# Kernel optimization log

Measured on AMD Instinct MI355X. Metric: run time of the kernel, lower is better.

The kernel has to match this reference:

```python
import jax, jax.numpy as jnp
import numpy as np

# ---- dims (from init_kwargs) ----
B_SZ = 16; K = 1; NC = 64; NR = 4; RF = 4; L_UL = 8
M_ANT = 256; N_ANT = 1024; BS_TDD = 16; RIS_TDD = 16
FC = 100e9; BW = 1e9; UPSNR = 10.0; MAX_DELAY = 5e-9; BIT = 1
C = NC  # PSA channel = Nc


def setup_inputs():
    key = jax.random.key(0)
    ks = jax.random.split(key, 20)
    f = jnp.float32
    d = {}
    d['H_BR_re'] = jax.random.normal(ks[0], (NC, N_ANT, M_ANT), f)
    d['H_BR_im'] = jax.random.normal(ks[1], (NC, N_ANT, M_ANT), f)
    d['H_RU_re'] = jax.random.normal(ks[2], (B_SZ, K, NC, NR, N_ANT), f)
    d['H_RU_im'] = jax.random.normal(ks[3], (B_SZ, K, NC, NR, N_ANT), f)
    d['H_BU_re'] = jax.random.normal(ks[4], (B_SZ, K, NC, NR, M_ANT), f)
    d['H_BU_im'] = jax.random.normal(ks[5], (B_SZ, K, NC, NR, M_ANT), f)
    # unit complex Gaussian noise, scaled by sqrt(Power*SNR/2) inside reference
    d['noise_re'] = jax.random.normal(ks[6], (B_SZ, L_UL, NC, NR, RF), f)
    d['noise_im'] = jax.random.normal(ks[7], (B_SZ, L_UL, NC, NR, RF), f)
    # learned parameters (torch: Parameter tensors in __init__)
    d['Phase1'] = jax.random.uniform(ks[8], (L_UL, N_ANT), f)
    d['Phase2'] = jax.random.uniform(ks[9], (L_UL, N_ANT), f)
    d['Phase_TDD'] = jax.random.normal(ks[10], (L_UL, RIS_TDD), f)
    d['S_analog'] = jax.random.normal(ks[11], (L_UL, NC, M_ANT, RF), f)
    d['S_analog_TDD'] = jax.random.normal(ks[12], (L_UL, NC, BS_TDD, RF), f)
    # ParallelPolarizedSelfAttention(channel=Nc) weights (1x1 convs -> [out,in])
    s = 0.05
    d['ch_wv_w'] = jax.random.normal(ks[13], (C // 2, C), f) * s
    d['ch_wv_b'] = jnp.zeros((C // 2,), f)
    d['ch_wq_w'] = jax.random.normal(ks[14], (1, C), f) * s
    d['ch_wq_b'] = jnp.zeros((1,), f)
    d['ch_wz_w'] = jax.random.normal(ks[15], (C, C // 2), f) * s
    d['ch_wz_b'] = jnp.zeros((C,), f)
    d['ln_w'] = jnp.ones((C,), f)
    d['ln_b'] = jnp.zeros((C,), f)
    d['sp_wv_w'] = jax.random.normal(ks[16], (C // 2, C), f) * s
    d['sp_wv_b'] = jnp.zeros((C // 2,), f)
    d['sp_wq_w'] = jax.random.normal(ks[17], (C // 2, C), f) * s
    d['sp_wq_b'] = jnp.zeros((C // 2,), f)
    return d


def _conv1x1(x, w, b):
    # 1x1 conv == channel mixing
    return jnp.einsum('bchw,oc->bohw', x, w) + b[None, :, None, None]


def _psa(x, ch_wv_w, ch_wv_b, ch_wq_w, ch_wq_b, ch_wz_w, ch_wz_b, ln_w, ln_b,
         sp_wv_w, sp_wv_b, sp_wq_w, sp_wq_b):
    # Parallel Polarized Self-Attention (channel branch + spatial branch)
    b, c, h, w = x.shape
    # channel-only self-attention
    cwv = _conv1x1(x, ch_wv_w, ch_wv_b).reshape(b, c // 2, h * w)
    cwq = jax.nn.softmax(_conv1x1(x, ch_wq_w, ch_wq_b).reshape(b, h * w), axis=1)
    cwz = jnp.einsum('bkn,bn->bk', cwv, cwq)          # [b, c//2]
    z = cwz @ ch_wz_w.T + ch_wz_b                      # [b, c]
    mu = jnp.mean(z, axis=-1, keepdims=True)
    var = jnp.var(z, axis=-1, keepdims=True)
    zn = (z - mu) / jnp.sqrt(var + 1e-5) * ln_w + ln_b  # LayerNorm over channel
    ch_weight = jax.nn.sigmoid(zn)[:, :, None, None]
    # spatial-only self-attention
    swv = _conv1x1(x, sp_wv_w, sp_wv_b).reshape(b, c // 2, h * w)
    swq = jax.nn.softmax(jnp.mean(_conv1x1(x, sp_wq_w, sp_wq_b), axis=(2, 3)), axis=-1)
    swz = jnp.einsum('bk,bkn->bn', swq, swv)
    sp_weight = jax.nn.sigmoid(swz.reshape(b, 1, h, w))
    return sp_weight * x + ch_weight * x


def reference(H_BR_re, H_BR_im, H_RU_re, H_RU_im, H_BU_re, H_BU_im,
              noise_re, noise_im, Phase1, Phase2, Phase_TDD, S_analog, S_analog_TDD,
              ch_wv_w, ch_wv_b, ch_wq_w, ch_wq_b, ch_wz_w, ch_wz_b, ln_w, ln_b,
              sp_wv_w, sp_wv_b, sp_wq_w, sp_wq_b):
    H_BR = H_BR_re + 1j * H_BR_im                       # [Nc, N_ant, M_ant]
    H_RU = H_RU_re[:, K - 1] + 1j * H_RU_im[:, K - 1]   # [B, Nc, Nr, N_ant]
    H_BU = H_BU_re[:, K - 1] + 1j * H_BU_im[:, K - 1]   # [B, Nc, Nr, M_ant]
    two_pi = 2.0 * jnp.pi
    # subcarrier frequencies fm = (n - (Nc+1)/2) * B/Nc + fc
    fm = ((jnp.arange(NC, dtype=jnp.float32) + 1.0) - (NC + 1) / 2.0) * (BW / NC) + FC
    # phase quantization (bit = 1 -> seg = pi)
    seg = two_pi / (2 ** BIT)
    th1 = jnp.exp(1j * (jnp.floor(two_pi * Phase1 / seg) * seg))  # [L, N_ant]
    th2 = jnp.exp(1j * (jnp.floor(two_pi * Phase2 / seg) * seg))  # [L, N_ant]
    # RIS true-time-delay phase, kron(Phi_T, ones(1, N_ant//RIS_TDD)) == repeat
    a1 = MAX_DELAY * jax.nn.sigmoid(Phase_TDD)                    # [L, RIS_TDD]
    phi_t = jnp.exp(1j * two_pi * fm[None, :, None] * a1[:, None, :])
    phi_tdd = jnp.repeat(phi_t, N_ANT // RIS_TDD, axis=-1)        # [L, Nc, N_ant]
    theta = th1[:, None, :] * phi_tdd * th2[:, None, :]           # diag(Theta) entries
    # BS analog precoder with TTDs; kron(S_T, ones(M//BS_TDD,1)) == row repeat
    S = jnp.exp(1j * S_analog) / float(np.sqrt(M_ANT))            # [L, Nc, M, RF]
    bdel = MAX_DELAY * jax.nn.sigmoid(S_analog_TDD)               # [L, Nc, BS_TDD, RF]
    s_t = jnp.exp(1j * two_pi * fm[None, :, None, None] * bdel)
    F = S * jnp.repeat(s_t, M_ANT // BS_TDD, axis=2)              # [L, Nc, M, RF]
    # H_RU @ diag(theta) == column-wise scaling (fused, no NxN diag matmul)
    scaled = H_RU[:, None] * theta[None, :, :, None, :]           # [B, L, Nc, Nr, N_ant]
    a = jnp.einsum('blcrn,cnm->blcrm', scaled, H_BR) + H_BU[:, None]
    y0 = jnp.einsum('blcrm,lcmf->blcrf', a, F)                    # [B, L, Nc, Nr, RF]
    power = jnp.sum(jnp.abs(y0) ** 2, axis=(3, 4))[..., None, None]
    snr_lin = 10.0 ** (-UPSNR / 10.0)
    noise = (noise_re + 1j * noise_im) * jnp.sqrt(power * snr_lin / 2.0)
    y = y0 + noise
    Y = jnp.transpose(y, (0, 2, 3, 4, 1)).reshape(B_SZ, NC, K * NR * RF, L_UL)
    x = jnp.concatenate([jnp.real(Y), jnp.imag(Y)], axis=3)       # [B, Nc, K*Nr*RF, 2L]
    return _psa(x, ch_wv_w, ch_wv_b, ch_wq_w, ch_wq_b, ch_wz_w, ch_wz_b,
                ln_w, ln_b, sp_wv_w, sp_wv_b, sp_wq_w, sp_wq_b)
```

## Files before the change

### kernel.cpp

```cpp
#include <hip/hip_runtime.h>
#include <math.h>

static constexpr double TWO_PI_D = 6.283185307179586476925287;

static constexpr size_t OFF_THRE = 0;
static constexpr size_t OFF_THIM = 524288;
static constexpr size_t OFF_FBF  = 1048576;
static constexpr size_t OFF_WTBF = 1572864;
static constexpr size_t OFF_Y0P  = 3670016;
static constexpr size_t OFF_X    = 4980736;
static constexpr size_t WS_FLOATS = 5242880;

typedef __attribute__((ext_vector_type(8))) short short8;
typedef __attribute__((ext_vector_type(4))) float f32x4;

__device__ __forceinline__ double fm_of(int c){
  return ((double)(c + 1) - 32.5) * (1.0e9 / 64.0) + 1.0e11;
}
__device__ __forceinline__ unsigned short f2bf(float x){
  unsigned int u = __float_as_uint(x);
  return (unsigned short)((u + 0x7FFFu + ((u >> 16) & 1u)) >> 16);
}

__global__ __launch_bounds__(256) void k_prep(
    const float* __restrict__ P1, const float* __restrict__ P2,
    const float* __restrict__ PT, const float* __restrict__ SA,
    const float* __restrict__ ST,
    float* __restrict__ tre, float* __restrict__ tim, unsigned short* __restrict__ Fbf)
{
  __shared__ double tcs[16], tsn[16];
  int bid = blockIdx.x, tid = threadIdx.x;
  const float TWO_PI_F = 6.2831855f, SEG_F = 3.1415927f;
  if (bid < 2048){
    int l = bid >> 8, c = (bid >> 2) & 63, n0 = (bid & 3) * 256;
    if (tid < 4){
      int ris = (n0 >> 6) + tid;
      double a1 = 5.0e-9 / (1.0 + exp((double)(-PT[l * 16 + ris])));
      sincos(TWO_PI_D * fm_of(c) * a1, &tsn[tid], &tcs[tid]);
    }
    __syncthreads();
    int n = n0 + tid;
    float p1 = P1[l * 1024 + n], p2 = P2[l * 1024 + n];
    int k1 = (int)floorf((TWO_PI_F * p1) / SEG_F);
    int k2 = (int)floorf((TWO_PI_F * p2) / SEG_F);
    float s = ((k1 + k2) & 1) ? -1.f : 1.f;
    int t = (l * 64 + c) * 1024 + n;
    int ti = tid >> 6;
    tre[t] = s * (float)tcs[ti];
    tim[t] = s * (float)tsn[ti];
  } else {
    int bid2 = bid - 2048;
    int l = bid2 >> 8, c = (bid2 >> 2) & 63, f = bid2 & 3;
    int m = tid;
    if (tid < 16){
      double bdel = 5.0e-9 / (1.0 + exp((double)(-ST[((l * 64 + c) * 16 + tid) * 4 + f])));
      sincos(TWO_PI_D * fm_of(c) * bdel, &tsn[tid], &tcs[tid]);
    }
    __syncthreads();
    float sa_ = SA[(size_t)((l * 64 + c) * 256 + m) * 4 + f];
    float ssa, csa;
    sincosf(sa_, &ssa, &csa);
    float cb = (float)tcs[m >> 4], sb = (float)tsn[m >> 4];
    size_t base = ((size_t)(c * 2) * 32 + (l * 4 + f)) * 256 + m;
    Fbf[base]        = f2bf((csa * cb - ssa * sb) * 0.0625f);
    Fbf[base + 8192] = f2bf((csa * sb + ssa * cb) * 0.0625f);
  }
}

__global__ __launch_bounds__(256) void k_W(
    const float* __restrict__ Hre, const float* __restrict__ Him,
    const unsigned short* __restrict__ Fbf,
    const float* __restrict__ tre, const float* __restrict__ tim,
    unsigned short* __restrict__ WTbf)
{
  const int bid = blockIdx.x;
  const int c = bid >> 4;
  const int n0 = (bid & 15) * 64;
  const int lane = threadIdx.x & 63, w = threadIdx.x >> 6;
  const int nt = n0 + w * 16;
  const int kq = lane >> 4, rm = lane & 15;

  const size_t arow = ((size_t)c * 1024 + nt + rm) * 256 + kq * 8;
  const float* hr = Hre + arow;
  const float* hi = Him + arow;
  const unsigned short* f0 = Fbf + (size_t)(c * 2) * 8192 + kq * 8;
  const unsigned short* fr0 = f0 + rm * 256;
  const unsigned short* fi0 = fr0 + 8192;
  const unsigned short* fr1 = f0 + (16 + rm) * 256;
  const unsigned short* fi1 = fr1 + 8192;

  f32x4 accRe0 = {0.f,0.f,0.f,0.f}, accIm0 = {0.f,0.f,0.f,0.f};
  f32x4 accRe1 = {0.f,0.f,0.f,0.f}, accIm1 = {0.f,0.f,0.f,0.f};

  #pragma unroll
  for (int ck = 0; ck < 8; ck++){
    const int mo = ck * 32;
    float4 r0 = *(const float4*)(hr + mo);
    float4 r1 = *(const float4*)(hr + mo + 4);
    float4 i0 = *(const float4*)(hi + mo);
    float4 i1 = *(const float4*)(hi + mo + 4);
    short8 bRe0 = *(const short8*)(fr0 + mo);
    short8 bIm0 = *(const short8*)(fi0 + mo);
    short8 bRe1 = *(const short8*)(fr1 + mo);
    short8 bIm1 = *(const short8*)(fi1 + mo);
    short8 are, aim;
    are[0]=(short)f2bf(r0.x); are[1]=(short)f2bf(r0.y); are[2]=(short)f2bf(r0.z); are[3]=(short)f2bf(r0.w);
    are[4]=(short)f2bf(r1.x); are[5]=(short)f2bf(r1.y); are[6]=(short)f2bf(r1.z); are[7]=(short)f2bf(r1.w);
    aim[0]=(short)f2bf(i0.x); aim[1]=(short)f2bf(i0.y); aim[2]=(short)f2bf(i0.z); aim[3]=(short)f2bf(i0.w);
    aim[4]=(short)f2bf(i1.x); aim[5]=(short)f2bf(i1.y); aim[6]=(short)f2bf(i1.z); aim[7]=(short)f2bf(i1.w);
    short8 bImN0, bImN1;
    #pragma unroll
    for (int j = 0; j < 8; j++){
      bImN0[j] = bIm0[j] ^ (short)0x8000;
      bImN1[j] = bIm1[j] ^ (short)0x8000;
    }
    accRe0 = __builtin_amdgcn_mfma_f32_16x16x32_bf16(are, bRe0,  accRe0, 0, 0, 0);
    accRe0 = __builtin_amdgcn_mfma_f32_16x16x32_bf16(aim, bImN0, accRe0, 0, 0, 0);
    accIm0 = __builtin_amdgcn_mfma_f32_16x16x32_bf16(are, bIm0,  accIm0, 0, 0, 0);
    accIm0 = __builtin_amdgcn_mfma_f32_16x16x32_bf16(aim, bRe0,  accIm0, 0, 0, 0);
    accRe1 = __builtin_amdgcn_mfma_f32_16x16x32_bf16(are, bRe1,  accRe1, 0, 0, 0);
    accRe1 = __builtin_amdgcn_mfma_f32_16x16x32_bf16(aim, bImN1, accRe1, 0, 0, 0);
    accIm1 = __builtin_amdgcn_mfma_f32_16x16x32_bf16(are, bIm1,  accIm1, 0, 0, 0);
    accIm1 = __builtin_amdgcn_mfma_f32_16x16x32_bf16(aim, bRe1,  accIm1, 0, 0, 0);
  }

  #pragma unroll
  for (int t = 0; t < 2; t++){
    const f32x4 aR = t ? accRe1 : accRe0;
    const f32x4 aI = t ? accIm1 : accIm0;
    int lf = t * 16 + rm;
    int l = lf >> 2;
    unsigned short pr[4], pi_[4];
    #pragma unroll
    for (int r = 0; r < 4; r++){
      size_t ti = (size_t)(l * 64 + c) * 1024 + nt + kq * 4 + r;
      float wr = tre[ti], wi = tim[ti];
      float xr = aR[r], xi = aI[r];
      pr[r]  = f2bf(wr * xr - wi * xi);
      pi_[r] = f2bf(wr * xi + wi * xr);
    }
    size_t rb = ((size_t)(c * 2) * 32 + lf) * 1024 + nt + kq * 4;
    *(uint2*)(WTbf + rb) =
        make_uint2((unsigned)pr[0] | ((unsigned)pr[1] << 16),
                   (unsigned)pr[2] | ((unsigned)pr[3] << 16));
    *(uint2*)(WTbf + rb + 32768) =
        make_uint2((unsigned)pi_[0] | ((unsigned)pi_[1] << 16),
                   (unsigned)pi_[2] | ((unsigned)pi_[3] << 16));
  }
}

__global__ __launch_bounds__(512) void k_y0(
    const float* __restrict__ Rre, const float* __restrict__ Rim,
    const float* __restrict__ Ure, const float* __restrict__ Uim,
    const unsigned short* __restrict__ WTbf, const unsigned short* __restrict__ Fbf,
    float* __restrict__ Y0p)
{
  __shared__ __align__(16) short lA[2][2][64][32];
  __shared__ __align__(16) short lB[2][2][32][32];
  const int bid = blockIdx.x;
  const int chunk = bid >> 6, c = bid & 63;
  const int tid = threadIdx.x;
  const int lane = tid & 63, w = tid >> 6;
  const int lftile = w & 1, mt = w >> 1;
  const int kq = lane >> 4, rm = lane & 15;
  const int s_mq = tid & 7, s_nr = tid >> 3;
  const int b_comp = tid >> 7, b_lf = (tid >> 2) & 31, b_q = tid & 3;

  const float* Are; const float* Aim; int ars, ac0;
  const unsigned short* Bb; int brs;
  if (chunk < 4){ Are = Rre; Aim = Rim; ars = 1024; ac0 = chunk * 256; Bb = WTbf; brs = 1024; }
  else          { Are = Ure; Aim = Uim; ars = 256;  ac0 = 0;           Bb = Fbf;  brs = 256;  }
  const size_t arow = ((size_t)((s_nr >> 2) * 64 + c) * 4 + (s_nr & 3)) * ars + ac0;

  f32x4 accRe = {0.f,0.f,0.f,0.f}, accIm = {0.f,0.f,0.f,0.f};
  float4 sRe, sIm; short8 sB;

  auto LOADC = [&](int ck){
    size_t g = arow + ck * 32 + s_mq * 4;
    sRe = *(const float4*)(Are + g);
    sIm = *(const float4*)(Aim + g);
    if (tid < 256){
      size_t gb = ((size_t)(c * 2 + b_comp) * 32 + b_lf) * brs + ac0 + ck * 32 + b_q * 8;
      sB = *(const short8*)(Bb + gb);
    }
  };
  auto WRITEC = [&](int buf){
    int eo = (((s_mq >> 1) ^ (s_nr & 3)) << 3) + (s_mq & 1) * 4;
    unsigned int r0 = (unsigned)f2bf(sRe.x) | ((unsigned)f2bf(sRe.y) << 16);
    unsigned int r1 = (unsigned)f2bf(sRe.z) | ((unsigned)f2bf(sRe.w) << 16);
    *(uint2*)&lA[buf][0][s_nr][eo] = make_uint2(r0, r1);
    unsigned int i0 = (unsigned)f2bf(sIm.x) | ((unsigned)f2bf(sIm.y) << 16);
    unsigned int i1 = (unsigned)f2bf(sIm.z) | ((unsigned)f2bf(sIm.w) << 16);
    *(uint2*)&lA[buf][1][s_nr][eo] = make_uint2(i0, i1);
    if (tid < 256){
      *(short8*)&lB[buf][b_comp][b_lf][(b_q ^ (b_lf & 3)) << 3] = sB;
    }
  };
  auto COMPUTE = [&](int buf){
    int col = lftile * 16 + rm;
    int be = (kq ^ (col & 3)) << 3;
    short8 bRe = *(const short8*)&lB[buf][0][col][be];
    short8 bIm = *(const short8*)&lB[buf][1][col][be];
    short8 bImN;
    #pragma unroll
    for (int i = 0; i < 8; i++) bImN[i] = bIm[i] ^ (short)0x8000;
    int row = mt * 16 + rm;
    int eo = (kq ^ (row & 3)) << 3;
    short8 are = *(const short8*)&lA[buf][0][row][eo];
    short8 aim = *(const short8*)&lA[buf][1][row][eo];
    accRe = __builtin_amdgcn_mfma_f32_16x16x32_bf16(are, bRe,  accRe, 0, 0, 0);
    accRe = __builtin_amdgcn_mfma_f32_16x16x32_bf16(aim, bImN, accRe, 0, 0, 0);
    accIm = __builtin_amdgcn_mfma_f32_16x16x32_bf16(are, bIm,  accIm, 0, 0, 0);
    accIm = __builtin_amdgcn_mfma_f32_16x16x32_bf16(aim, bRe,  accIm, 0, 0, 0);
  };

  LOADC(0); WRITEC(0); __syncthreads();
  for (int ck = 0; ck < 8; ck++){
    int buf = ck & 1;
    if (ck < 7) LOADC(ck + 1);
    COMPUTE(buf);
    if (ck < 7) WRITEC(buf ^ 1);
    __syncthreads();
  }

  #pragma unroll
  for (int r = 0; r < 4; r++){
    int row = mt * 16 + kq * 4 + r;
    int lf = lftile * 16 + rm;
    size_t idx = ((size_t)(chunk * 64 + c) * 64 + row) * 32 + lf;
    float2 o; o.x = accRe[r]; o.y = accIm[r];
    *(float2*)(Y0p + idx * 2) = o;
  }
}

__global__ __launch_bounds__(256) void k_fin(
    const float* __restrict__ Y0p,
    const float* __restrict__ nre, const float* __restrict__ nim,
    float* __restrict__ X)
{
  int wid = blockIdx.x * 4 + (threadIdx.x >> 6);
  int lane = threadIdx.x & 63;
  int c = wid & 63, l = (wid >> 6) & 7, b = wid >> 9;
  int pair = lane >> 2;
  int r = pair >> 2, f = pair & 3;
  float yR = 0.f, yI = 0.f;
  #pragma unroll
  for (int ch = 0; ch < 5; ch++){
    size_t idx = ((size_t)(ch * 64 + c) * 64 + b * 4 + r) * 32 + l * 4 + f;
    float2 v = *(const float2*)(Y0p + idx * 2);
    yR += v.x; yI += v.y;
  }
  float p = yR * yR + yI * yI;
  p += __shfl_xor(p, 4); p += __shfl_xor(p, 8);
  p += __shfl_xor(p, 16); p += __shfl_xor(p, 32);
  float sc = sqrtf(p * 0.05f);
  if ((lane & 3) == 0){
    size_t ni = ((size_t)((b * 8 + l) * 64 + c) * 4 + r) * 4 + f;
    float oR = yR + nre[ni] * sc;
    float oI = yI + nim[ni] * sc;
    size_t xb = ((size_t)(b * 64 + c) * 16 + pair) * 16;
    X[xb + l]     = oR;
    X[xb + 8 + l] = oI;
  }
}

__global__ __launch_bounds__(256) void k_psa(
    const float* __restrict__ Xin,
    const float* __restrict__ wv_w, const float* __restrict__ wv_b,
    const float* __restrict__ wq_w, const float* __restrict__ wq_b,
    const float* __restrict__ wz_w, const float* __restrict__ wz_b,
    const float* __restrict__ lnw, const float* __restrict__ lnb,
    const float* __restrict__ sv_w, const float* __restrict__ sv_b,
    const float* __restrict__ sq_w, const float* __restrict__ sq_b,
    float* __restrict__ out)
{
  __shared__ float x[64 * 257];
  __shared__ float buf[256];
  __shared__ float xms[64], xqs[64], chw[64], wcomb[64];
  __shared__ float cwzs[32], swqs[32];
  __shared__ float red4[8];
  int b = blockIdx.x, tid = threadIdx.x;
  const float* xin = Xin + (size_t)b * 16384;
  for (int kk = 0; kk < 64; kk++){
    int i = tid + 256 * kk;
    x[(i >> 8) * 257 + (i & 255)] = xin[i];
  }
  __syncthreads();
  if (tid < 64){
    float s = 0.f;
    for (int n = 0; n < 256; n++) s += x[tid * 257 + n];
    xms[tid] = s * (1.f / 256.f);
  }
  float lq = wq_b[0];
  for (int cc = 0; cc < 64; cc++) lq += wq_w[cc] * x[cc * 257 + tid];
  float mx = lq;
  for (int s = 1; s < 64; s <<= 1) mx = fmaxf(mx, __shfl_xor(mx, s));
  if ((tid & 63) == 0) red4[tid >> 6] = mx;
  __syncthreads();
  mx = fmaxf(fmaxf(red4[0], red4[1]), fmaxf(red4[2], red4[3]));
  float e = expf(lq - mx);
  float se = e;
  for (int s = 1; s < 64; s <<= 1) se += __shfl_xor(se, s);
  if ((tid & 63) == 0) red4[4 + (tid >> 6)] = se;
  __syncthreads();
  se = red4[4] + red4[5] + red4[6] + red4[7];
  buf[tid] = e / se;
  __syncthreads();
  if (tid < 64){
    float s = 0.f;
    for (int n = 0; n < 256; n++) s += x[tid * 257 + n] * buf[n];
    xqs[tid] = s;
  }
  __syncthreads();
  if (tid < 32){
    float s = wv_b[tid];
    for (int cc = 0; cc < 64; cc++) s += wv_w[tid * 64 + cc] * xqs[cc];
    cwzs[tid] = s;
  }
  __syncthreads();
  if (tid < 64){
    float z = wz_b[tid];
    for (int k = 0; k < 32; k++) z += cwzs[k] * wz_w[tid * 32 + k];
    float s1 = z, s2 = z * z;
    for (int s = 1; s < 64; s <<= 1){ s1 += __shfl_xor(s1, s); s2 += __shfl_xor(s2, s); }
    float mu = s1 * (1.f / 64.f);
    float var = s2 * (1.f / 64.f) - mu * mu;
    float zn = (z - mu) * rsqrtf(var + 1e-5f) * lnw[tid] + lnb[tid];
    chw[tid] = 1.f / (1.f + expf(-zn));
  }
  if (tid < 32){
    float s = sq_b[tid];
    for (int cc = 0; cc < 64; cc++) s += sq_w[tid * 64 + cc] * xms[cc];
    float m2 = s;
    for (int st = 1; st < 32; st <<= 1) m2 = fmaxf(m2, __shfl_xor(m2, st));
    float ee = expf(s - m2), ss = ee;
    for (int st = 1; st < 32; st <<= 1) ss += __shfl_xor(ss, st);
    swqs[tid] = ee / ss;
  }
  __syncthreads();
  if (tid < 64){
    float s = 0.f;
    for (int k = 0; k < 32; k++) s += swqs[k] * sv_w[k * 64 + tid];
    wcomb[tid] = s;
  }
  __syncthreads();
  float bcomb = 0.f;
  for (int k = 0; k < 32; k++) bcomb += swqs[k] * sv_b[k];
  float sz = bcomb;
  for (int cc = 0; cc < 64; cc++) sz += wcomb[cc] * x[cc * 257 + tid];
  float spw = 1.f / (1.f + expf(-sz));
  buf[tid] = spw;
  __syncthreads();
  for (int kk = 0; kk < 64; kk++){
    int i = tid + 256 * kk;
    int cc = i >> 8, n = i & 255;
    out[(size_t)b * 16384 + i] = (buf[n] + chw[cc]) * x[cc * 257 + n];
  }
}

extern "C" void kernel_launch(void* const* d_in, const int* in_sizes, int n_in,
                              void* d_out, int out_size, void* d_ws, size_t ws_size,
                              hipStream_t stream)
{
  if (ws_size < WS_FLOATS * sizeof(float)) return;
  const float* HBRre = (const float*)d_in[0];
  const float* HBRim = (const float*)d_in[1];
  const float* HRUre = (const float*)d_in[2];
  const float* HRUim = (const float*)d_in[3];
  const float* HBUre = (const float*)d_in[4];
  const float* HBUim = (const float*)d_in[5];
  const float* nre   = (const float*)d_in[6];
  const float* nim   = (const float*)d_in[7];
  const float* P1    = (const float*)d_in[8];
  const float* P2    = (const float*)d_in[9];
  const float* PT    = (const float*)d_in[10];
  const float* SA    = (const float*)d_in[11];
  const float* ST    = (const float*)d_in[12];
  const float* wv_w  = (const float*)d_in[13];
  const float* wv_b  = (const float*)d_in[14];
  const float* wq_w  = (const float*)d_in[15];
  const float* wq_b  = (const float*)d_in[16];
  const float* wz_w  = (const float*)d_in[17];
  const float* wz_b  = (const float*)d_in[18];
  const float* lnw   = (const float*)d_in[19];
  const float* lnb   = (const float*)d_in[20];
  const float* sv_w  = (const float*)d_in[21];
  const float* sv_b  = (const float*)d_in[22];
  const float* sq_w  = (const float*)d_in[23];
  const float* sq_b  = (const float*)d_in[24];

  float* ws  = (float*)d_ws;
  float* tre = ws + OFF_THRE;
  float* tim = ws + OFF_THIM;
  unsigned short* fbf  = (unsigned short*)(ws + OFF_FBF);
  unsigned short* wtbf = (unsigned short*)(ws + OFF_WTBF);
  float* y0p = ws + OFF_Y0P;
  float* xb  = ws + OFF_X;

  k_prep<<<4096, 256, 0, stream>>>(P1, P2, PT, SA, ST, tre, tim, fbf);
  k_W<<<1024, 256, 0, stream>>>(HBRre, HBRim, fbf, tre, tim, wtbf);
  k_y0<<<320, 512, 0, stream>>>(HRUre, HRUim, HBUre, HBUim, wtbf, fbf, y0p);
  k_fin<<<2048, 256, 0, stream>>>(y0p, nre, nim, xb);
  k_psa<<<16, 256, 0, stream>>>(xb, wv_w, wv_b, wq_w, wq_b, wz_w, wz_b,
                                lnw, lnb, sv_w, sv_b, sq_w, sq_b, (float*)d_out);
}
```

Baseline: 69.98 us.

## Split k_W work per wave across lf tiles and double-buffer K loads

Each wave in k_W now computes a single 16-wide lf tile instead of two, so H rows are shared by two waves and the grid doubles to 2048 blocks over 32-row n chunks. The K loop is hand-pipelined with two register buffer sets, issuing the next chunk's loads before the current chunk's MFMAs. The goal is more parallelism and latency hiding on the memory-bound H_BR read. The cost is that each H_BR element is loaded twice, once per lf tile, which relies on cache to avoid doubling global traffic.

Result: slower. 83.17 us (+18.8%).

```diff
diff --git a/kernel.cpp b/kernel.cpp
--- a/kernel.cpp
+++ b/kernel.cpp
@@ -74,68 +74,81 @@
     unsigned short* __restrict__ WTbf)
 {
   const int bid = blockIdx.x;
-  const int c = bid >> 4;
-  const int n0 = (bid & 15) * 64;
+  const int c = bid >> 5;
+  const int n0 = (bid & 31) * 32;
   const int lane = threadIdx.x & 63, w = threadIdx.x >> 6;
-  const int nt = n0 + w * 16;
+  const int lftile = w & 1, rh = w >> 1;
+  const int nt = n0 + rh * 16;
   const int kq = lane >> 4, rm = lane & 15;
+  const int lf = lftile * 16 + rm;
 
   const size_t arow = ((size_t)c * 1024 + nt + rm) * 256 + kq * 8;
   const float* hr = Hre + arow;
   const float* hi = Him + arow;
-  const unsigned short* f0 = Fbf + (size_t)(c * 2) * 8192 + kq * 8;
-  const unsigned short* fr0 = f0 + rm * 256;
-  const unsigned short* fi0 = fr0 + 8192;
-  const unsigned short* fr1 = f0 + (16 + rm) * 256;
-  const unsigned short* fi1 = fr1 + 8192;
-
-  f32x4 accRe0 = {0.f,0.f,0.f,0.f}, accIm0 = {0.f,0.f,0.f,0.f};
-  f32x4 accRe1 = {0.f,0.f,0.f,0.f}, accIm1 = {0.f,0.f,0.f,0.f};
-
-  #pragma unroll
-  for (int ck = 0; ck < 8; ck++){
-    const int mo = ck * 32;
-    float4 r0 = *(const float4*)(hr + mo);
-    float4 r1 = *(const float4*)(hr + mo + 4);
-    float4 i0 = *(const float4*)(hi + mo);
-    float4 i1 = *(const float4*)(hi + mo + 4);
-    short8 bRe0 = *(const short8*)(fr0 + mo);
-    short8 bIm0 = *(const short8*)(fi0 + mo);
-    short8 bRe1 = *(const short8*)(fr1 + mo);
-    short8 bIm1 = *(const short8*)(fi1 + mo);
-    short8 are, aim;
-    are[0]=(short)f2bf(r0.x); are[1]=(short)f2bf(r0.y); are[2]=(short)f2bf(r0.z); are[3]=(short)f2bf(r0.w);
-    are[4]=(short)f2bf(r1.x); are[5]=(short)f2bf(r1.y); are[6]=(short)f2bf(r1.z); are[7]=(short)f2bf(r1.w);
-    aim[0]=(short)f2bf(i0.x); aim[1]=(short)f2bf(i0.y); aim[2]=(short)f2bf(i0.z); aim[3]=(short)f2bf(i0.w);
-    aim[4]=(short)f2bf(i1.x); aim[5]=(short)f2bf(i1.y); aim[6]=(short)f2bf(i1.z); aim[7]=(short)f2bf(i1.w);
-    short8 bImN0, bImN1;
-    #pragma unroll
-    for (int j = 0; j < 8; j++){
-      bImN0[j] = bIm0[j] ^ (short)0x8000;
-      bImN1[j] = bIm1[j] ^ (short)0x8000;
-    }
-    accRe0 = __builtin_amdgcn_mfma_f32_16x16x32_bf16(are, bRe0,  accRe0, 0, 0, 0);
-    accRe0 = __builtin_amdgcn_mfma_f32_16x16x32_bf16(aim, bImN0, accRe0, 0, 0, 0);
-    accIm0 = __builtin_amdgcn_mfma_f32_16x16x32_bf16(are, bIm0,  accIm0, 0, 0, 0);
-    accIm0 = __builtin_amdgcn_mfma_f32_16x16x32_bf16(aim, bRe0,  accIm0, 0, 0, 0);
-    accRe1 = __builtin_amdgcn_mfma_f32_16x16x32_bf16(are, bRe1,  accRe1, 0, 0, 0);
-    accRe1 = __builtin_amdgcn_mfma_f32_16x16x32_bf16(aim, bImN1, accRe1, 0, 0, 0);
-    accIm1 = __builtin_amdgcn_mfma_f32_16x16x32_bf16(are, bIm1,  accIm1, 0, 0, 0);
-    accIm1 = __builtin_amdgcn_mfma_f32_16x16x32_bf16(aim, bRe1,  accIm1, 0, 0, 0);
-  }
-
-  #pragma unroll
-  for (int t = 0; t < 2; t++){
-    const f32x4 aR = t ? accRe1 : accRe0;
-    const f32x4 aI = t ? accIm1 : accIm0;
-    int lf = t * 16 + rm;
-    int l = lf >> 2;
+  const unsigned short* fr = Fbf + (size_t)c * 16384 + (size_t)lf * 256 + kq * 8;
+  const unsigned short* fi = fr + 8192;
+
+  f32x4 accRe = {0.f,0.f,0.f,0.f}, accIm = {0.f,0.f,0.f,0.f};
+
+  float4 r0A, r1A, i0A, i1A; short8 brA, biA;
+  float4 r0B, r1B, i0B, i1B; short8 brB, biB;
+
+#define LOADK(S, CK) do {                              \
+    const int mo_ = (CK) * 32;                         \
+    r0##S = *(const float4*)(hr + mo_);                \
+    r1##S = *(const float4*)(hr + mo_ + 4);            \
+    i0##S = *(const float4*)(hi + mo_);                \
+    i1##S = *(const float4*)(hi + mo_ + 4);            \
+    br##S = *(const short8*)(fr + mo_);                \
+    bi##S = *(const short8*)(fi + mo_);                \
+  } while (0)
+
+#define COMPK(S) do {                                                                 \
+    short8 are_, aim_, bin_;                                                          \
+    are_[0]=(short)f2bf(r0##S.x); are_[1]=(short)f2bf(r0##S.y);                       \
+    are_[2]=(short)f2bf(r0##S.z); are_[3]=(short)f2bf(r0##S.w);                       \
+    are_[4]=(short)f2bf(r1##S.x); are_[5]=(short)f2bf(r1##S.y);                       \
+    are_[6]=(short)f2bf(r1##S.z); are_[7]=(short)f2bf(r1##S.w);                       \
+    aim_[0]=(short)f2bf(i0##S.x); aim_[1]=(short)f2bf(i0##S.y);                       \
+    aim_[2]=(short)f2bf(i0##S.z); aim_[3]=(short)f2bf(i0##S.w);                       \
+    aim_[4]=(short)f2bf(i1##S.x); aim_[5]=(short)f2bf(i1##S.y);                       \
+    aim_[6]=(short)f2bf(i1##S.z); aim_[7]=(short)f2bf(i1##S.w);                       \
+    _Pragma("unroll")                                                                 \
+    for (int j = 0; j < 8; j++) bin_[j] = bi##S[j] ^ (short)0x8000;                   \
+    accRe = __builtin_amdgcn_mfma_f32_16x16x32_bf16(are_, br##S, accRe, 0, 0, 0);     \
+    accRe = __builtin_amdgcn_mfma_f32_16x16x32_bf16(aim_, bin_,  accRe, 0, 0, 0);     \
+    accIm = __builtin_amdgcn_mfma_f32_16x16x32_bf16(are_, bi##S, accIm, 0, 0, 0);     \
+    accIm = __builtin_amdgcn_mfma_f32_16x16x32_bf16(aim_, br##S, accIm, 0, 0, 0);     \
+  } while (0)
+
+  LOADK(A, 0);
+  LOADK(B, 1);
+  COMPK(A);
+  LOADK(A, 2);
+  COMPK(B);
+  LOADK(B, 3);
+  COMPK(A);
+  LOADK(A, 4);
+  COMPK(B);
+  LOADK(B, 5);
+  COMPK(A);
+  LOADK(A, 6);
+  COMPK(B);
+  LOADK(B, 7);
+  COMPK(A);
+  COMPK(B);
+
+#undef LOADK
+#undef COMPK
+
+  {
+    const int l = lf >> 2;
     unsigned short pr[4], pi_[4];
     #pragma unroll
     for (int r = 0; r < 4; r++){
       size_t ti = (size_t)(l * 64 + c) * 1024 + nt + kq * 4 + r;
       float wr = tre[ti], wi = tim[ti];
-      float xr = aR[r], xi = aI[r];
+      float xr = accRe[r], xi = accIm[r];
       pr[r]  = f2bf(wr * xr - wi * xi);
       pi_[r] = f2bf(wr * xi + wi * xr);
     }
@@ -398,7 +411,7 @@
   float* xb  = ws + OFF_X;
 
   k_prep<<<4096, 256, 0, stream>>>(P1, P2, PT, SA, ST, tre, tim, fbf);
-  k_W<<<1024, 256, 0, stream>>>(HBRre, HBRim, fbf, tre, tim, wtbf);
+  k_W<<<2048, 256, 0, stream>>>(HBRre, HBRim, fbf, tre, tim, wtbf);
   k_y0<<<320, 512, 0, stream>>>(HRUre, HRUim, HBUre, HBUim, wtbf, fbf, y0p);
   k_fin<<<2048, 256, 0, stream>>>(y0p, nre, nim, xb);
   k_psa<<<16, 256, 0, stream>>>(xb, wv_w, wv_b, wq_w, wq_b, wz_w, wz_b,
```

## Stage H_BR tile in LDS via direct global-to-LDS loads and retile k_W

Applied to the files above, without the earlier changes.

k_W now copies each block's 32-row slab of H_BR real/imag (fp32) into padded shared memory with global_load_lds, then has each wave compute one 16x16 output tile from LDS. The block tile shrinks to 32 rows and the grid doubles, with two blocks per CU requested. The aim is coalesced, asynchronous streaming of the large H_BR read, plus more parallelism. In exchange each wave does half the MFMA work per A-load, and LDS use (about 65 KB per block) limits occupancy.

After: 72.09 us. 3.0% more time.

```diff
diff --git a/kernel.cpp b/kernel.cpp
--- a/kernel.cpp
+++ b/kernel.cpp
@@ -13,6 +13,8 @@
 
 typedef __attribute__((ext_vector_type(8))) short short8;
 typedef __attribute__((ext_vector_type(4))) float f32x4;
+typedef __attribute__((address_space(3))) unsigned int lds_u32;
+typedef const __attribute__((address_space(1))) unsigned int glo_u32;
 
 __device__ __forceinline__ double fm_of(int c){
   return ((double)(c + 1) - 32.5) * (1.0e9 / 64.0) + 1.0e11;
@@ -67,75 +69,73 @@
   }
 }
 
-__global__ __launch_bounds__(256) void k_W(
+__global__ __launch_bounds__(256, 2) void k_W(
     const float* __restrict__ Hre, const float* __restrict__ Him,
     const unsigned short* __restrict__ Fbf,
     const float* __restrict__ tre, const float* __restrict__ tim,
     unsigned short* __restrict__ WTbf)
 {
+  __shared__ __align__(16) float lA[16640];
   const int bid = blockIdx.x;
-  const int c = bid >> 4;
-  const int n0 = (bid & 15) * 64;
-  const int lane = threadIdx.x & 63, w = threadIdx.x >> 6;
-  const int nt = n0 + w * 16;
+  const int c = bid >> 5;
+  const int n0 = (bid & 31) * 32;
+  const int tid = threadIdx.x;
+  const int lane = tid & 63, w = tid >> 6;
+
+  const float* hre0 = Hre + ((size_t)c * 1024 + n0) * 256;
+  const float* him0 = Him + ((size_t)c * 1024 + n0) * 256;
+  #pragma unroll
+  for (int i = 0; i < 16; i++){
+    int t = w * 16 + i;
+    int row = t & 31;
+    const float* src = ((t >> 5) ? him0 : hre0) + (size_t)row * 256 + (lane << 2);
+    __builtin_amdgcn_global_load_lds((glo_u32*)src, (lds_u32*)&lA[t * 260], 16, 0, 0);
+  }
+  __syncthreads();
+
+  const int lftile = w & 1, rowhalf = w >> 1;
   const int kq = lane >> 4, rm = lane & 15;
-
-  const size_t arow = ((size_t)c * 1024 + nt + rm) * 256 + kq * 8;
-  const float* hr = Hre + arow;
-  const float* hi = Him + arow;
-  const unsigned short* f0 = Fbf + (size_t)(c * 2) * 8192 + kq * 8;
-  const unsigned short* fr0 = f0 + rm * 256;
-  const unsigned short* fi0 = fr0 + 8192;
-  const unsigned short* fr1 = f0 + (16 + rm) * 256;
-  const unsigned short* fi1 = fr1 + 8192;
-
-  f32x4 accRe0 = {0.f,0.f,0.f,0.f}, accIm0 = {0.f,0.f,0.f,0.f};
-  f32x4 accRe1 = {0.f,0.f,0.f,0.f}, accIm1 = {0.f,0.f,0.f,0.f};
+  const int lf = lftile * 16 + rm;
+  const int rrow = rowhalf * 16 + rm;
+  const int nt = n0 + rowhalf * 16;
+
+  const float* aRe = &lA[rrow * 260 + kq * 8];
+  const float* aIm = aRe + 32 * 260;
+  const unsigned short* fr = Fbf + (size_t)c * 16384 + (size_t)lf * 256 + kq * 8;
+  const unsigned short* fi = fr + 8192;
+
+  f32x4 accRe = {0.f,0.f,0.f,0.f}, accIm = {0.f,0.f,0.f,0.f};
 
   #pragma unroll
   for (int ck = 0; ck < 8; ck++){
     const int mo = ck * 32;
-    float4 r0 = *(const float4*)(hr + mo);
-    float4 r1 = *(const float4*)(hr + mo + 4);
-    float4 i0 = *(const float4*)(hi + mo);
-    float4 i1 = *(const float4*)(hi + mo + 4);
-    short8 bRe0 = *(const short8*)(fr0 + mo);
-    short8 bIm0 = *(const short8*)(fi0 + mo);
-    short8 bRe1 = *(const short8*)(fr1 + mo);
-    short8 bIm1 = *(const short8*)(fi1 + mo);
-    short8 are, aim;
+    float4 r0 = *(const float4*)(aRe + mo);
+    float4 r1 = *(const float4*)(aRe + mo + 4);
+    float4 i0 = *(const float4*)(aIm + mo);
+    float4 i1 = *(const float4*)(aIm + mo + 4);
+    short8 bre = *(const short8*)(fr + mo);
+    short8 bim = *(const short8*)(fi + mo);
+    short8 are, aim, bin;
     are[0]=(short)f2bf(r0.x); are[1]=(short)f2bf(r0.y); are[2]=(short)f2bf(r0.z); are[3]=(short)f2bf(r0.w);
     are[4]=(short)f2bf(r1.x); are[5]=(short)f2bf(r1.y); are[6]=(short)f2bf(r1.z); are[7]=(short)f2bf(r1.w);
     aim[0]=(short)f2bf(i0.x); aim[1]=(short)f2bf(i0.y); aim[2]=(short)f2bf(i0.z); aim[3]=(short)f2bf(i0.w);
     aim[4]=(short)f2bf(i1.x); aim[5]=(short)f2bf(i1.y); aim[6]=(short)f2bf(i1.z); aim[7]=(short)f2bf(i1.w);
-    short8 bImN0, bImN1;
     #pragma unroll
-    for (int j = 0; j < 8; j++){
-      bImN0[j] = bIm0[j] ^ (short)0x8000;
-      bImN1[j] = bIm1[j] ^ (short)0x8000;
-    }
-    accRe0 = __builtin_amdgcn_mfma_f32_16x16x32_bf16(are, bRe0,  accRe0, 0, 0, 0);
-    accRe0 = __builtin_amdgcn_mfma_f32_16x16x32_bf16(aim, bImN0, accRe0, 0, 0, 0);
-    accIm0 = __builtin_amdgcn_mfma_f32_16x16x32_bf16(are, bIm0,  accIm0, 0, 0, 0);
-    accIm0 = __builtin_amdgcn_mfma_f32_16x16x32_bf16(aim, bRe0,  accIm0, 0, 0, 0);
-    accRe1 = __builtin_amdgcn_mfma_f32_16x16x32_bf16(are, bRe1,  accRe1, 0, 0, 0);
-    accRe1 = __builtin_amdgcn_mfma_f32_16x16x32_bf16(aim, bImN1, accRe1, 0, 0, 0);
-    accIm1 = __builtin_amdgcn_mfma_f32_16x16x32_bf16(are, bIm1,  accIm1, 0, 0, 0);
-    accIm1 = __builtin_amdgcn_mfma_f32_16x16x32_bf16(aim, bRe1,  accIm1, 0, 0, 0);
-  }
-
-  #pragma unroll
-  for (int t = 0; t < 2; t++){
-    const f32x4 aR = t ? accRe1 : accRe0;
-    const f32x4 aI = t ? accIm1 : accIm0;
-    int lf = t * 16 + rm;
-    int l = lf >> 2;
+    for (int j = 0; j < 8; j++) bin[j] = bim[j] ^ (short)0x8000;
+    accRe = __builtin_amdgcn_mfma_f32_16x16x32_bf16(are, bre, accRe, 0, 0, 0);
+    accRe = __builtin_amdgcn_mfma_f32_16x16x32_bf16(aim, bin, accRe, 0, 0, 0);
+    accIm = __builtin_amdgcn_mfma_f32_16x16x32_bf16(are, bim, accIm, 0, 0, 0);
+    accIm = __builtin_amdgcn_mfma_f32_16x16x32_bf16(aim, bre, accIm, 0, 0, 0);
+  }
+
+  {
+    const int l = lf >> 2;
     unsigned short pr[4], pi_[4];
     #pragma unroll
     for (int r = 0; r < 4; r++){
       size_t ti = (size_t)(l * 64 + c) * 1024 + nt + kq * 4 + r;
       float wr = tre[ti], wi = tim[ti];
-      float xr = aR[r], xi = aI[r];
+      float xr = accRe[r], xi = accIm[r];
       pr[r]  = f2bf(wr * xr - wi * xi);
       pi_[r] = f2bf(wr * xi + wi * xr);
     }
@@ -398,7 +398,7 @@
   float* xb  = ws + OFF_X;
 
   k_prep<<<4096, 256, 0, stream>>>(P1, P2, PT, SA, ST, tre, tim, fbf);
-  k_W<<<1024, 256, 0, stream>>>(HBRre, HBRim, fbf, tre, tim, wtbf);
+  k_W<<<2048, 256, 0, stream>>>(HBRre, HBRim, fbf, tre, tim, wtbf);
   k_y0<<<320, 512, 0, stream>>>(HRUre, HRUim, HBUre, HBUim, wtbf, fbf, y0p);
   k_fin<<<2048, 256, 0, stream>>>(y0p, nre, nim, xb);
   k_psa<<<16, 256, 0, stream>>>(xb, wv_w, wv_b, wq_w, wq_b, wz_w, wz_b,
```

## Stage F tile in LDS and software-pipeline H loads in k_W

Applied to the files above, without the earlier changes.

The k_W kernel now copies the per-channel bf16 F tile into padded shared memory once per block, replacing the repeated per-wave global loads. It also issues the fp32 H row loads through inline asm with a three-stage prefetch ring, using explicit vmcnt waits so global memory latency overlaps the bf16 conversion and MFMA work. It adds an occupancy hint of 4 blocks per CU. The cost is about 33KB of LDS per block, a barrier, and fragile hand-scheduled waitcnt logic that must stay in sync with the load count.

Result: no change. 69.72 us (-0.4%).

```diff
diff --git a/kernel.cpp b/kernel.cpp
--- a/kernel.cpp
+++ b/kernel.cpp
@@ -67,62 +67,96 @@
   }
 }
 
-__global__ __launch_bounds__(256) void k_W(
+__global__ __launch_bounds__(256, 4) void k_W(
     const float* __restrict__ Hre, const float* __restrict__ Him,
     const unsigned short* __restrict__ Fbf,
     const float* __restrict__ tre, const float* __restrict__ tim,
     unsigned short* __restrict__ WTbf)
 {
+  __shared__ __align__(16) char lF[2 * 16896];
   const int bid = blockIdx.x;
   const int c = bid >> 4;
-  const int n0 = (bid & 15) * 64;
-  const int lane = threadIdx.x & 63, w = threadIdx.x >> 6;
-  const int nt = n0 + w * 16;
+  const int nt = (bid & 15) * 64 + (threadIdx.x >> 6) * 16;
+  const int lane = threadIdx.x & 63;
   const int kq = lane >> 4, rm = lane & 15;
 
-  const size_t arow = ((size_t)c * 1024 + nt + rm) * 256 + kq * 8;
-  const float* hr = Hre + arow;
-  const float* hi = Him + arow;
-  const unsigned short* f0 = Fbf + (size_t)(c * 2) * 8192 + kq * 8;
-  const unsigned short* fr0 = f0 + rm * 256;
-  const unsigned short* fi0 = fr0 + 8192;
-  const unsigned short* fr1 = f0 + (16 + rm) * 256;
-  const unsigned short* fi1 = fr1 + 8192;
-
-  f32x4 accRe0 = {0.f,0.f,0.f,0.f}, accIm0 = {0.f,0.f,0.f,0.f};
-  f32x4 accRe1 = {0.f,0.f,0.f,0.f}, accIm1 = {0.f,0.f,0.f,0.f};
-
-  #pragma unroll
-  for (int ck = 0; ck < 8; ck++){
-    const int mo = ck * 32;
-    float4 r0 = *(const float4*)(hr + mo);
-    float4 r1 = *(const float4*)(hr + mo + 4);
-    float4 i0 = *(const float4*)(hi + mo);
-    float4 i1 = *(const float4*)(hi + mo + 4);
-    short8 bRe0 = *(const short8*)(fr0 + mo);
-    short8 bIm0 = *(const short8*)(fi0 + mo);
-    short8 bRe1 = *(const short8*)(fr1 + mo);
-    short8 bIm1 = *(const short8*)(fi1 + mo);
-    short8 are, aim;
-    are[0]=(short)f2bf(r0.x); are[1]=(short)f2bf(r0.y); are[2]=(short)f2bf(r0.z); are[3]=(short)f2bf(r0.w);
-    are[4]=(short)f2bf(r1.x); are[5]=(short)f2bf(r1.y); are[6]=(short)f2bf(r1.z); are[7]=(short)f2bf(r1.w);
-    aim[0]=(short)f2bf(i0.x); aim[1]=(short)f2bf(i0.y); aim[2]=(short)f2bf(i0.z); aim[3]=(short)f2bf(i0.w);
-    aim[4]=(short)f2bf(i1.x); aim[5]=(short)f2bf(i1.y); aim[6]=(short)f2bf(i1.z); aim[7]=(short)f2bf(i1.w);
-    short8 bImN0, bImN1;
+  {
+    const unsigned short* fb = Fbf + (size_t)c * 16384;
     #pragma unroll
-    for (int j = 0; j < 8; j++){
-      bImN0[j] = bIm0[j] ^ (short)0x8000;
-      bImN1[j] = bIm1[j] ^ (short)0x8000;
-    }
-    accRe0 = __builtin_amdgcn_mfma_f32_16x16x32_bf16(are, bRe0,  accRe0, 0, 0, 0);
-    accRe0 = __builtin_amdgcn_mfma_f32_16x16x32_bf16(aim, bImN0, accRe0, 0, 0, 0);
-    accIm0 = __builtin_amdgcn_mfma_f32_16x16x32_bf16(are, bIm0,  accIm0, 0, 0, 0);
-    accIm0 = __builtin_amdgcn_mfma_f32_16x16x32_bf16(aim, bRe0,  accIm0, 0, 0, 0);
-    accRe1 = __builtin_amdgcn_mfma_f32_16x16x32_bf16(are, bRe1,  accRe1, 0, 0, 0);
-    accRe1 = __builtin_amdgcn_mfma_f32_16x16x32_bf16(aim, bImN1, accRe1, 0, 0, 0);
-    accIm1 = __builtin_amdgcn_mfma_f32_16x16x32_bf16(are, bIm1,  accIm1, 0, 0, 0);
-    accIm1 = __builtin_amdgcn_mfma_f32_16x16x32_bf16(aim, bRe1,  accIm1, 0, 0, 0);
-  }
+    for (int kk = 0; kk < 8; kk++){
+      int idx = kk * 256 + threadIdx.x;
+      int comp = idx >> 10, lf = (idx >> 5) & 31, gm = idx & 31;
+      short8 v = *(const short8*)(fb + comp * 8192 + lf * 256 + gm * 8);
+      *(short8*)(lF + comp * 16896 + lf * 528 + gm * 16) = v;
+    }
+  }
+  __syncthreads();
+
+  const float* hr = Hre + ((size_t)c * 1024 + nt + rm) * 256 + kq * 8;
+  const float* hi = Him + ((size_t)c * 1024 + nt + rm) * 256 + kq * 8;
+  const char* fb0 = lF + rm * 528 + kq * 16;
+  const char* fb1 = fb0 + 16 * 528;
+
+  float4 pR0[3], pR1[3], pI0[3], pI1[3];
+  f32x4 accRe0 = {0,0,0,0}, accIm0 = {0,0,0,0};
+  f32x4 accRe1 = {0,0,0,0}, accIm1 = {0,0,0,0};
+
+#define ISS(S, OA, OB) do{                                                \
+    asm volatile("global_load_dwordx4 %0, %2, off offset:" OA "\n\t"      \
+                 "global_load_dwordx4 %1, %2, off offset:" OB             \
+      : "=&v"(pR0[S]), "=&v"(pR1[S]) : "v"(hr));                          \
+    asm volatile("global_load_dwordx4 %0, %2, off offset:" OA "\n\t"      \
+                 "global_load_dwordx4 %1, %2, off offset:" OB             \
+      : "=&v"(pI0[S]), "=&v"(pI1[S]) : "v"(hi));                          \
+  }while(0)
+
+#define WAITC(N) do{                                                      \
+    asm volatile("s_waitcnt vmcnt(" N ")" ::: "memory");                  \
+    __builtin_amdgcn_sched_barrier(0);                                    \
+  }while(0)
+
+#define COMP(S, CK) do{                                                                  \
+    short8 bRe0 = *(const short8*)(fb0 + (CK) * 64);                                     \
+    short8 bIm0 = *(const short8*)(fb0 + 16896 + (CK) * 64);                             \
+    short8 bRe1 = *(const short8*)(fb1 + (CK) * 64);                                     \
+    short8 bIm1 = *(const short8*)(fb1 + 16896 + (CK) * 64);                             \
+    short8 are, aim, bin0, bin1;                                                         \
+    are[0]=(short)f2bf(pR0[S].x); are[1]=(short)f2bf(pR0[S].y);                          \
+    are[2]=(short)f2bf(pR0[S].z); are[3]=(short)f2bf(pR0[S].w);                          \
+    are[4]=(short)f2bf(pR1[S].x); are[5]=(short)f2bf(pR1[S].y);                          \
+    are[6]=(short)f2bf(pR1[S].z); are[7]=(short)f2bf(pR1[S].w);                          \
+    aim[0]=(short)f2bf(pI0[S].x); aim[1]=(short)f2bf(pI0[S].y);                          \
+    aim[2]=(short)f2bf(pI0[S].z); aim[3]=(short)f2bf(pI0[S].w);                          \
+    aim[4]=(short)f2bf(pI1[S].x); aim[5]=(short)f2bf(pI1[S].y);                          \
+    aim[6]=(short)f2bf(pI1[S].z); aim[7]=(short)f2bf(pI1[S].w);                          \
+    _Pragma("unroll")                                                                    \
+    for (int j = 0; j < 8; j++){ bin0[j] = bIm0[j] ^ (short)0x8000;                      \
+                                 bin1[j] = bIm1[j] ^ (short)0x8000; }                    \
+    accRe0 = __builtin_amdgcn_mfma_f32_16x16x32_bf16(are, bRe0, accRe0, 0, 0, 0);        \
+    accRe0 = __builtin_amdgcn_mfma_f32_16x16x32_bf16(aim, bin0, accRe0, 0, 0, 0);        \
+    accIm0 = __builtin_amdgcn_mfma_f32_16x16x32_bf16(are, bIm0, accIm0, 0, 0, 0);        \
+    accIm0 = __builtin_amdgcn_mfma_f32_16x16x32_bf16(aim, bRe0, accIm0, 0, 0, 0);        \
+    accRe1 = __builtin_amdgcn_mfma_f32_16x16x32_bf16(are, bRe1, accRe1, 0, 0, 0);        \
+    accRe1 = __builtin_amdgcn_mfma_f32_16x16x32_bf16(aim, bin1, accRe1, 0, 0, 0);        \
+    accIm1 = __builtin_amdgcn_mfma_f32_16x16x32_bf16(are, bIm1, accIm1, 0, 0, 0);        \
+    accIm1 = __builtin_amdgcn_mfma_f32_16x16x32_bf16(aim, bRe1, accIm1, 0, 0, 0);        \
+  }while(0)
+
+  ISS(0, "0",   "16");
+  ISS(1, "128", "144");
+  ISS(2, "256", "272");
+  WAITC("8"); COMP(0, 0); ISS(0, "384", "400");
+  WAITC("8"); COMP(1, 1); ISS(1, "512", "528");
+  WAITC("8"); COMP(2, 2); ISS(2, "640", "656");
+  WAITC("8"); COMP(0, 3); ISS(0, "768", "784");
+  WAITC("8"); COMP(1, 4); ISS(1, "896", "912");
+  WAITC("8"); COMP(2, 5);
+  WAITC("4"); COMP(0, 6);
+  WAITC("0"); COMP(1, 7);
+
+#undef ISS
+#undef WAITC
+#undef COMP
 
   #pragma unroll
   for (int t = 0; t < 2; t++){
```
